# Optimization experiments

Measured on AMD Instinct MI355X. Metric: run time of the kernel, lower is better.

## Reference

```python
import jax, jax.numpy as jnp
import numpy as np

N_EMBED = 1024
N_HEAD = 16

def setup_inputs() -> dict:
    key = jax.random.key(0)
    ks = jax.random.split(key, 5)
    C = N_EMBED
    x = jax.random.normal(ks[0], (2, 2048, C), dtype=jnp.float32)
    # nn.Linear default init scale ~ 1/sqrt(fan_in)
    W_attn = jax.random.normal(ks[1], (C, 3 * C), dtype=jnp.float32) / np.sqrt(C)
    b_attn = jax.random.normal(ks[2], (3 * C,), dtype=jnp.float32) / np.sqrt(C)
    W_out = jax.random.normal(ks[3], (C, C), dtype=jnp.float32) / np.sqrt(C)
    b_out = jax.random.normal(ks[4], (C,), dtype=jnp.float32) / np.sqrt(C)
    return {"x": x, "W_attn": W_attn, "b_attn": b_attn, "W_out": W_out, "b_out": b_out}

def reference(x, W_attn, b_attn, W_out, b_out):
    B, T, C = x.shape
    H = N_HEAD
    D = C // H  # head dim
    qkv = x @ W_attn + b_attn  # [B,T,3C]
    q, k, v = jnp.split(qkv, 3, axis=2)
    # [B,T,C] -> [B,H,T,D]
    q = q.reshape(B, T, H, D).transpose(0, 2, 1, 3)
    k = k.reshape(B, T, H, D).transpose(0, 2, 1, 3)
    v = v.reshape(B, T, H, D).transpose(0, 2, 1, 3)
    scale = 1.0 / np.sqrt(D).astype(np.float32)
    att = jnp.einsum('bhqd,bhkd->bhqk', q, k) * scale  # [B,H,T,T]
    causal = jnp.tril(jnp.ones((T, T), dtype=bool))
    att = jnp.where(causal[None, None, :, :], att, -jnp.inf)
    wei = jax.nn.softmax(att, axis=-1)
    out = jnp.einsum('bhqk,bhkd->bhqd', wei, v)  # [B,H,T,D]
    out = out.transpose(0, 2, 1, 3).reshape(B, T, C)
    return out @ W_out + b_out
```

## Files before the change

kernel.cpp:

```cpp
#include <hip/hip_runtime.h>
#include <hip/hip_bf16.h>

typedef __attribute__((ext_vector_type(8))) short bf16x8;
typedef __attribute__((ext_vector_type(4))) float f32x4;

#define DI __device__ __forceinline__

DI short f2bf(float f) {
  __hip_bfloat16 b = __float2bfloat16(f);
  return __builtin_bit_cast(short, b);
}

DI void g2l16(const void* g, void* l) {
  __builtin_amdgcn_global_load_lds(
      (const __attribute__((address_space(1))) unsigned int*)g,
      (__attribute__((address_space(3))) unsigned int*)l, 16, 0, 0);
}

DI f32x4 mfma16(bf16x8 a, bf16x8 b, f32x4 c) {
  return __builtin_amdgcn_mfma_f32_16x16x32_bf16(a, b, c, 0, 0, 0);
}

__global__ void k_cvt(const float* __restrict__ in, short* __restrict__ out, int n4) {
  int i = blockIdx.x * blockDim.x + threadIdx.x;
  if (i >= n4) return;
  float4 v = reinterpret_cast<const float4*>(in)[i];
  short4 o;
  o.x = f2bf(v.x); o.y = f2bf(v.y); o.z = f2bf(v.z); o.w = f2bf(v.w);
  reinterpret_cast<short4*>(out)[i] = o;
}

__global__ void k_tr_w(const float* __restrict__ in, short* __restrict__ out,
                       int rows, int cols) {
  __shared__ float t[32][33];
  int c0 = blockIdx.x * 32, r0 = blockIdx.y * 32;
  int tx = threadIdx.x & 31, ty = threadIdx.x >> 5;
  #pragma unroll
  for (int i = ty; i < 32; i += 8) t[i][tx] = in[(size_t)(r0 + i) * cols + c0 + tx];
  __syncthreads();
  #pragma unroll
  for (int i = ty; i < 32; i += 8)
    out[(size_t)(c0 + i) * rows + r0 + tx] = f2bf(t[tx][i]);
}

__global__ void k_tr_v(const short* __restrict__ qkv, short* __restrict__ vt) {
  __shared__ short t[32][33];
  int b = blockIdx.z;
  int t0 = blockIdx.x * 32, c0 = blockIdx.y * 32;
  int tx = threadIdx.x & 31, ty = threadIdx.x >> 5;
  #pragma unroll
  for (int i = ty; i < 32; i += 8)
    t[i][tx] = qkv[(size_t)(b * 2048 + t0 + i) * 3072 + 2048 + c0 + tx];
  __syncthreads();
  #pragma unroll
  for (int i = ty; i < 32; i += 8)
    vt[((size_t)(b * 1024 + c0 + i)) * 2048 + t0 + tx] = t[tx][i];
}

template <int OUT_F32>
__global__ __launch_bounds__(256, 2)
void k_gemm_bt(const short* __restrict__ A, const short* __restrict__ Bt,
               const float* __restrict__ bias, void* __restrict__ Cout,
               int M, int N, int K) {
  __shared__ short As[128 * 32];
  __shared__ short Bs[128 * 32];
  const int tid = threadIdx.x;
  const int wid = tid >> 6, lane = tid & 63;
  const int g = lane >> 4, c = lane & 15;
  const int row0 = blockIdx.x * 128, col0 = blockIdx.y * 128;
  const int wr = wid >> 1, wc = wid & 1;
  f32x4 acc[4][4] = {};

  const int sR = lane >> 2;
  const int sp = lane & 3;

  for (int kt = 0; kt < K; kt += 32) {
    #pragma unroll
    for (int i = 0; i < 2; ++i) {
      int R = wid * 32 + i * 16 + sR;
      int cc = sp ^ ((R >> 1) & 3);
      g2l16(A  + (size_t)(row0 + R) * K + kt + cc * 8, &As[(wid * 32 + i * 16) * 32]);
      g2l16(Bt + (size_t)(col0 + R) * K + kt + cc * 8, &Bs[(wid * 32 + i * 16) * 32]);
    }
    __syncthreads();
    bf16x8 af[4], bf[4];
    #pragma unroll
    for (int mi = 0; mi < 4; ++mi) {
      int r = wr * 64 + mi * 16 + c;
      int pc = g ^ ((r >> 1) & 3);
      af[mi] = *(const bf16x8*)&As[r * 32 + pc * 8];
    }
    #pragma unroll
    for (int ni = 0; ni < 4; ++ni) {
      int r = wc * 64 + ni * 16 + c;
      int pc = g ^ ((r >> 1) & 3);
      bf[ni] = *(const bf16x8*)&Bs[r * 32 + pc * 8];
    }
    #pragma unroll
    for (int mi = 0; mi < 4; ++mi)
      #pragma unroll
      for (int ni = 0; ni < 4; ++ni)
        acc[mi][ni] = mfma16(af[mi], bf[ni], acc[mi][ni]);
    __syncthreads();
  }

  #pragma unroll
  for (int mi = 0; mi < 4; ++mi) {
    int r = row0 + wr * 64 + mi * 16 + g * 4;
    #pragma unroll
    for (int ni = 0; ni < 4; ++ni) {
      int cg = col0 + wc * 64 + ni * 16 + c;
      float bv = bias[cg];
      #pragma unroll
      for (int q = 0; q < 4; ++q) {
        float v = acc[mi][ni][q] + bv;
        if (OUT_F32) ((float*)Cout)[(size_t)(r + q) * N + cg] = v;
        else         ((short*)Cout)[(size_t)(r + q) * N + cg] = f2bf(v);
      }
    }
  }
}

__global__ __launch_bounds__(512, 1)
void k_attn(const short* __restrict__ qkv, const short* __restrict__ vt,
            short* __restrict__ att) {
  constexpr int T = 2048, C3 = 3072, Cc = 1024;
  __shared__ short Ks[2][64 * 64];
  __shared__ short Vs[2][64 * 64];
  __shared__ short Pb[8][32 * 64];
  const int tid = threadIdx.x, wid = tid >> 6, lane = tid & 63;
  const int g = lane >> 4, c = lane & 15;
  const int bh = blockIdx.y, b = bh >> 4, h = bh & 15;
  const int p = blockIdx.x;
  const int grp = wid >> 2;
  const int wl = wid & 3;
  const int qt = grp ? (15 - p) : p;
  const int q0 = qt * 128;
  const int qrow = q0 + wl * 32;
  const int nsteps = 2 * (16 - p);

  bf16x8 qf[2][2];
  #pragma unroll
  for (int mi = 0; mi < 2; ++mi)
    #pragma unroll
    for (int kd = 0; kd < 2; ++kd)
      qf[mi][kd] = *(const bf16x8*)(qkv + (size_t)(b * T + qrow + mi * 16 + c) * C3
                                    + h * 64 + kd * 32 + g * 8);

  f32x4 oacc[2][4] = {};
  float lsum[2][4];
  #pragma unroll
  for (int mi = 0; mi < 2; ++mi)
    #pragma unroll
    for (int r = 0; r < 4; ++r) lsum[mi][r] = 0.f;

  const int sR = lane >> 3, sp = lane & 7;
  const int stR = wid * 8 + sR;
  const int scc = sp ^ (stR & 7);
  const short* ksrc = qkv + (size_t)b * T * C3 + Cc + h * 64 + scc * 8 + (size_t)stR * C3;
  const short* vsrc = vt + ((size_t)(b * Cc + h * 64 + stR)) * T + scc * 8;

  auto STAGE = [&](int t) {
    int kt = t * 64;
    int bufi = t & 1;
    g2l16(ksrc + (size_t)kt * C3, &Ks[bufi][(wid * 8) * 64]);
    g2l16(vsrc + kt,              &Vs[bufi][(wid * 8) * 64]);
  };

  STAGE(0);
  __syncthreads();

  for (int t = 0; t < nsteps; ++t) {
    if (t + 1 < nsteps) STAGE(t + 1);
    const int kt = t * 64;
    const short* Kb = Ks[t & 1];
    const short* Vb = Vs[t & 1];

    if (kt <= qrow + 31) {
      f32x4 s[2][4] = {};
      #pragma unroll
      for (int kd = 0; kd < 2; ++kd) {
        #pragma unroll
        for (int ni = 0; ni < 4; ++ni) {
          int r = ni * 16 + c;
          int pc = (kd * 4 + g) ^ (r & 7);
          bf16x8 kf = *(const bf16x8*)&Kb[r * 64 + pc * 8];
          #pragma unroll
          for (int mi = 0; mi < 2; ++mi)
            s[mi][ni] = mfma16(qf[mi][kd], kf, s[mi][ni]);
        }
      }
      constexpr float c1 = 0.125f * 1.44269504f;
      constexpr float c2 = 16.0f * 1.44269504f;
      #pragma unroll
      for (int mi = 0; mi < 2; ++mi)
        #pragma unroll
        for (int ni = 0; ni < 4; ++ni) {
          int kg = kt + ni * 16 + c;
          #pragma unroll
          for (int r = 0; r < 4; ++r) {
            int qg = qrow + mi * 16 + g * 4 + r;
            float arg = (kg <= qg) ? fmaf(s[mi][ni][r], c1, -c2) : -1000.0f;
            s[mi][ni][r] = exp2f(arg);
          }
        }
      #pragma unroll
      for (int mi = 0; mi < 2; ++mi)
        #pragma unroll
        for (int r = 0; r < 4; ++r) {
          float rs = s[mi][0][r] + s[mi][1][r] + s[mi][2][r] + s[mi][3][r];
          #pragma unroll
          for (int off = 1; off < 16; off <<= 1) rs += __shfl_xor(rs, off);
          lsum[mi][r] += rs;
        }
      #pragma unroll
      for (int mi = 0; mi < 2; ++mi)
        #pragma unroll
        for (int ni = 0; ni < 4; ++ni)
          #pragma unroll
          for (int r = 0; r < 4; ++r) {
            int row = mi * 16 + g * 4 + r;
            int col = ni * 16 + c;
            int pc = (col >> 3) ^ (row & 7);
            Pb[wid][row * 64 + pc * 8 + (col & 7)] = f2bf(s[mi][ni][r]);
          }
      #pragma unroll
      for (int kk = 0; kk < 2; ++kk) {
        bf16x8 pf[2];
        #pragma unroll
        for (int mi = 0; mi < 2; ++mi) {
          int row = mi * 16 + c;
          int pc = (kk * 4 + g) ^ (row & 7);
          pf[mi] = *(const bf16x8*)&Pb[wid][row * 64 + pc * 8];
        }
        #pragma unroll
        for (int ni = 0; ni < 4; ++ni) {
          int row = ni * 16 + c;
          int pc = (kk * 4 + g) ^ (row & 7);
          bf16x8 vf = *(const bf16x8*)&Vb[row * 64 + pc * 8];
          #pragma unroll
          for (int mi = 0; mi < 2; ++mi)
            oacc[mi][ni] = mfma16(pf[mi], vf, oacc[mi][ni]);
        }
      }
    }
    __syncthreads();
  }

  float inv[2][4];
  #pragma unroll
  for (int mi = 0; mi < 2; ++mi)
    #pragma unroll
    for (int r = 0; r < 4; ++r) inv[mi][r] = 1.f / lsum[mi][r];
  #pragma unroll
  for (int mi = 0; mi < 2; ++mi)
    #pragma unroll
    for (int ni = 0; ni < 4; ++ni)
      #pragma unroll
      for (int r = 0; r < 4; ++r) {
        int qg = qrow + mi * 16 + g * 4 + r;
        att[(size_t)(b * T + qg) * Cc + h * 64 + ni * 16 + c] =
            f2bf(oacc[mi][ni][r] * inv[mi][r]);
      }
}

extern "C" void kernel_launch(void* const* d_in, const int* in_sizes, int n_in,
                              void* d_out, int out_size, void* d_ws, size_t ws_size,
                              hipStream_t stream) {
  (void)in_sizes; (void)n_in; (void)out_size; (void)ws_size;
  const float* x  = (const float*)d_in[0];
  const float* Wa = (const float*)d_in[1];
  const float* ba = (const float*)d_in[2];
  const float* Wo = (const float*)d_in[3];
  const float* bo = (const float*)d_in[4];
  float* out = (float*)d_out;

  short* xb  = (short*)d_ws;
  short* Wat = xb  + (size_t)4096 * 1024;
  short* Wot = Wat + (size_t)3072 * 1024;
  short* qkv = Wot + (size_t)1024 * 1024;
  short* vtb = qkv + (size_t)4096 * 3072;
  short* att = xb;

  k_cvt<<<4096, 256, 0, stream>>>(x, xb, 4096 * 1024 / 4);
  k_tr_w<<<dim3(96, 32), 256, 0, stream>>>(Wa, Wat, 1024, 3072);
  k_tr_w<<<dim3(32, 32), 256, 0, stream>>>(Wo, Wot, 1024, 1024);
  k_gemm_bt<0><<<dim3(32, 24), 256, 0, stream>>>(xb, Wat, ba, qkv, 4096, 3072, 1024);
  k_tr_v<<<dim3(64, 32, 2), 256, 0, stream>>>(qkv, vtb);
  k_attn<<<dim3(8, 32), 512, 0, stream>>>(qkv, vtb, att);
  k_gemm_bt<1><<<dim3(32, 8), 256, 0, stream>>>(att, Wot, bo, out, 4096, 1024, 1024);
}
```

Before: 225.0 us.

## Fold softmax scale into QKV GEMM and transpose score layout in attention

The QKV GEMM epilogue now multiplies the Q columns by the softmax scale times log2(e), so the attention loop no longer needs a per-element FMA and drops the fixed -16 exponent offset. Scores are computed transposed (K as the A operand), so each lane holds a query column: the row-sum needs two shuffles instead of four, and P is packed with v_cvt_pk_bf16_f32 and written to LDS as 64-bit stores. The causal mask is applied only on diagonal tiles, and exp2 goes through the hardware builtin. Dropping the max offset means large scores could overflow exp2, and rounding scaled Q to bf16 slightly changes numerics.

```diff
diff --git a/kernel.cpp b/kernel.cpp
--- a/kernel.cpp
+++ b/kernel.cpp
@@ -5,6 +5,12 @@
 typedef __attribute__((ext_vector_type(4))) float f32x4;
 
 #define DI __device__ __forceinline__
+
+#if __has_builtin(__builtin_amdgcn_exp2f)
+#define EXP2(x) __builtin_amdgcn_exp2f(x)
+#else
+#define EXP2(x) exp2f(x)
+#endif
 
 DI short f2bf(float f) {
   __hip_bfloat16 b = __float2bfloat16(f);
@@ -61,7 +67,7 @@
 __global__ __launch_bounds__(256, 2)
 void k_gemm_bt(const short* __restrict__ A, const short* __restrict__ Bt,
                const float* __restrict__ bias, void* __restrict__ Cout,
-               int M, int N, int K) {
+               int M, int N, int K, int qn, float qs) {
   __shared__ short As[128 * 32];
   __shared__ short Bs[128 * 32];
   const int tid = threadIdx.x;
@@ -111,9 +117,10 @@
     for (int ni = 0; ni < 4; ++ni) {
       int cg = col0 + wc * 64 + ni * 16 + c;
       float bv = bias[cg];
+      float sc = (cg < qn) ? qs : 1.0f;
       #pragma unroll
       for (int q = 0; q < 4; ++q) {
-        float v = acc[mi][ni][q] + bv;
+        float v = (acc[mi][ni][q] + bv) * sc;
         if (OUT_F32) ((float*)Cout)[(size_t)(r + q) * N + cg] = v;
         else         ((short*)Cout)[(size_t)(r + q) * N + cg] = f2bf(v);
       }
@@ -127,7 +134,7 @@
   constexpr int T = 2048, C3 = 3072, Cc = 1024;
   __shared__ short Ks[2][64 * 64];
   __shared__ short Vs[2][64 * 64];
-  __shared__ short Pb[8][32 * 64];
+  __shared__ unsigned int PbU[8][32 * 32];
   const int tid = threadIdx.x, wid = tid >> 6, lane = tid & 63;
   const int g = lane >> 4, c = lane & 15;
   const int bh = blockIdx.y, b = bh >> 4, h = bh & 15;
@@ -148,11 +155,7 @@
                                     + h * 64 + kd * 32 + g * 8);
 
   f32x4 oacc[2][4] = {};
-  float lsum[2][4];
-  #pragma unroll
-  for (int mi = 0; mi < 2; ++mi)
-    #pragma unroll
-    for (int r = 0; r < 4; ++r) lsum[mi][r] = 0.f;
+  float lsum[2] = {0.f, 0.f};
 
   const int sR = lane >> 3, sp = lane & 7;
   const int stR = wid * 8 + sR;
@@ -170,6 +173,8 @@
   STAGE(0);
   __syncthreads();
 
+  unsigned int* pb = &PbU[wid][0];
+
   for (int t = 0; t < nsteps; ++t) {
     if (t + 1 < nsteps) STAGE(t + 1);
     const int kt = t * 64;
@@ -177,90 +182,105 @@
     const short* Vb = Vs[t & 1];
 
     if (kt <= qrow + 31) {
-      f32x4 s[2][4] = {};
+      f32x4 s[4][2] = {};
       #pragma unroll
       for (int kd = 0; kd < 2; ++kd) {
         #pragma unroll
         for (int ni = 0; ni < 4; ++ni) {
-          int r = ni * 16 + c;
-          int pc = (kd * 4 + g) ^ (r & 7);
-          bf16x8 kf = *(const bf16x8*)&Kb[r * 64 + pc * 8];
+          int rr = ni * 16 + c;
+          int pc = (kd * 4 + g) ^ (rr & 7);
+          bf16x8 kf = *(const bf16x8*)&Kb[rr * 64 + pc * 8];
           #pragma unroll
           for (int mi = 0; mi < 2; ++mi)
-            s[mi][ni] = mfma16(qf[mi][kd], kf, s[mi][ni]);
+            s[ni][mi] = mfma16(kf, qf[mi][kd], s[ni][mi]);
         }
       }
-      constexpr float c1 = 0.125f * 1.44269504f;
-      constexpr float c2 = 16.0f * 1.44269504f;
-      #pragma unroll
-      for (int mi = 0; mi < 2; ++mi)
-        #pragma unroll
-        for (int ni = 0; ni < 4; ++ni) {
-          int kg = kt + ni * 16 + c;
-          #pragma unroll
-          for (int r = 0; r < 4; ++r) {
-            int qg = qrow + mi * 16 + g * 4 + r;
-            float arg = (kg <= qg) ? fmaf(s[mi][ni][r], c1, -c2) : -1000.0f;
-            s[mi][ni][r] = exp2f(arg);
-          }
-        }
-      #pragma unroll
-      for (int mi = 0; mi < 2; ++mi)
-        #pragma unroll
-        for (int r = 0; r < 4; ++r) {
-          float rs = s[mi][0][r] + s[mi][1][r] + s[mi][2][r] + s[mi][3][r];
-          #pragma unroll
-          for (int off = 1; off < 16; off <<= 1) rs += __shfl_xor(rs, off);
-          lsum[mi][r] += rs;
-        }
-      #pragma unroll
-      for (int mi = 0; mi < 2; ++mi)
+      if (kt + 63 > qrow) {
         #pragma unroll
         for (int ni = 0; ni < 4; ++ni)
           #pragma unroll
           for (int r = 0; r < 4; ++r) {
-            int row = mi * 16 + g * 4 + r;
-            int col = ni * 16 + c;
-            int pc = (col >> 3) ^ (row & 7);
-            Pb[wid][row * 64 + pc * 8 + (col & 7)] = f2bf(s[mi][ni][r]);
+            int kg = kt + ni * 16 + g * 4 + r;
+            #pragma unroll
+            for (int mi = 0; mi < 2; ++mi) {
+              int qg = qrow + mi * 16 + c;
+              if (kg > qg) s[ni][mi][r] = -1000.0f;
+            }
           }
+      }
+      #pragma unroll
+      for (int ni = 0; ni < 4; ++ni)
+        #pragma unroll
+        for (int mi = 0; mi < 2; ++mi)
+          #pragma unroll
+          for (int r = 0; r < 4; ++r)
+            s[ni][mi][r] = EXP2(s[ni][mi][r]);
+      #pragma unroll
+      for (int mi = 0; mi < 2; ++mi) {
+        float rs = 0.f;
+        #pragma unroll
+        for (int ni = 0; ni < 4; ++ni)
+          rs += (s[ni][mi][0] + s[ni][mi][1]) + (s[ni][mi][2] + s[ni][mi][3]);
+        rs += __shfl_xor(rs, 16);
+        rs += __shfl_xor(rs, 32);
+        lsum[mi] += rs;
+      }
+      #pragma unroll
+      for (int mi = 0; mi < 2; ++mi) {
+        int q = mi * 16 + c;
+        int rowb = q * 32;
+        int sw = q & 7;
+        #pragma unroll
+        for (int ni = 0; ni < 4; ++ni) {
+          unsigned int p0, p1;
+          asm("v_cvt_pk_bf16_f32 %0, %1, %2"
+              : "=v"(p0) : "v"(s[ni][mi][0]), "v"(s[ni][mi][1]));
+          asm("v_cvt_pk_bf16_f32 %0, %1, %2"
+              : "=v"(p1) : "v"(s[ni][mi][2]), "v"(s[ni][mi][3]));
+          int idx = rowb + ((2 * ni + (g >> 1)) ^ sw) * 4 + 2 * (g & 1);
+          uint2 w2; w2.x = p0; w2.y = p1;
+          *reinterpret_cast<uint2*>(&pb[idx]) = w2;
+        }
+      }
       #pragma unroll
       for (int kk = 0; kk < 2; ++kk) {
-        bf16x8 pf[2];
+        bf16x8 vf[4];
+        #pragma unroll
+        for (int nd = 0; nd < 4; ++nd) {
+          int rr = nd * 16 + c;
+          int pc = (kk * 4 + g) ^ (rr & 7);
+          vf[nd] = *(const bf16x8*)&Vb[rr * 64 + pc * 8];
+        }
         #pragma unroll
         for (int mi = 0; mi < 2; ++mi) {
-          int row = mi * 16 + c;
-          int pc = (kk * 4 + g) ^ (row & 7);
-          pf[mi] = *(const bf16x8*)&Pb[wid][row * 64 + pc * 8];
-        }
-        #pragma unroll
-        for (int ni = 0; ni < 4; ++ni) {
-          int row = ni * 16 + c;
-          int pc = (kk * 4 + g) ^ (row & 7);
-          bf16x8 vf = *(const bf16x8*)&Vb[row * 64 + pc * 8];
+          int q = mi * 16 + c;
+          bf16x8 pa = *(const bf16x8*)&pb[q * 32 + ((4 * kk + g) ^ (q & 7)) * 4];
           #pragma unroll
-          for (int mi = 0; mi < 2; ++mi)
-            oacc[mi][ni] = mfma16(pf[mi], vf, oacc[mi][ni]);
+          for (int nd = 0; nd < 4; ++nd)
+            oacc[mi][nd] = mfma16(pa, vf[nd], oacc[mi][nd]);
         }
       }
     }
     __syncthreads();
   }
 
-  float inv[2][4];
+  float* Lw = reinterpret_cast<float*>(pb);
+  if (g == 0) { Lw[c] = lsum[0]; Lw[16 + c] = lsum[1]; }
+  f32x4 l0 = *reinterpret_cast<const f32x4*>(&Lw[g * 4]);
+  f32x4 l1 = *reinterpret_cast<const f32x4*>(&Lw[16 + g * 4]);
+  f32x4 inv[2];
+  #pragma unroll
+  for (int r = 0; r < 4; ++r) { inv[0][r] = 1.0f / l0[r]; inv[1][r] = 1.0f / l1[r]; }
+
   #pragma unroll
   for (int mi = 0; mi < 2; ++mi)
     #pragma unroll
-    for (int r = 0; r < 4; ++r) inv[mi][r] = 1.f / lsum[mi][r];
-  #pragma unroll
-  for (int mi = 0; mi < 2; ++mi)
-    #pragma unroll
-    for (int ni = 0; ni < 4; ++ni)
+    for (int nd = 0; nd < 4; ++nd)
       #pragma unroll
       for (int r = 0; r < 4; ++r) {
         int qg = qrow + mi * 16 + g * 4 + r;
-        att[(size_t)(b * T + qg) * Cc + h * 64 + ni * 16 + c] =
-            f2bf(oacc[mi][ni][r] * inv[mi][r]);
+        att[(size_t)(b * T + qg) * Cc + h * 64 + nd * 16 + c] =
+            f2bf(oacc[mi][nd][r] * inv[mi][r]);
       }
 }
 
@@ -282,11 +302,15 @@
   short* vtb = qkv + (size_t)4096 * 3072;
   short* att = xb;
 
+  const float QS = 0.125f * 1.44269504f;
+
   k_cvt<<<4096, 256, 0, stream>>>(x, xb, 4096 * 1024 / 4);
   k_tr_w<<<dim3(96, 32), 256, 0, stream>>>(Wa, Wat, 1024, 3072);
   k_tr_w<<<dim3(32, 32), 256, 0, stream>>>(Wo, Wot, 1024, 1024);
-  k_gemm_bt<0><<<dim3(32, 24), 256, 0, stream>>>(xb, Wat, ba, qkv, 4096, 3072, 1024);
+  k_gemm_bt<0><<<dim3(32, 24), 256, 0, stream>>>(xb, Wat, ba, qkv, 4096, 3072, 1024,
+                                                 1024, QS);
   k_tr_v<<<dim3(64, 32, 2), 256, 0, stream>>>(qkv, vtb);
   k_attn<<<dim3(8, 32), 512, 0, stream>>>(qkv, vtb, att);
-  k_gemm_bt<1><<<dim3(32, 8), 256, 0, stream>>>(att, Wot, bo, out, 4096, 1024, 1024);
-}
+  k_gemm_bt<1><<<dim3(32, 8), 256, 0, stream>>>(att, Wot, bo, out, 4096, 1024, 1024,
+                                                0, 1.0f);
+}
```

Result: faster. 197.0 us (-12.5%).
